# Performance work log

Hardware: AMD Instinct MI355X
Metric: run time of the kernel (lower is better)

The kernel has to match this reference:

```python
import jax, jax.numpy as jnp
import numpy as np

N_NODES = 100000
N_EDGES = 800000
NUM_GRAPHS = 64


def _lin_init(key, fan_in, fan_out):
    k1, k2 = jax.random.split(key)
    s = 1.0 / np.sqrt(fan_in)
    W = jax.random.uniform(k1, (fan_in, fan_out), jnp.float32, -s, s)
    b = jax.random.uniform(k2, (fan_out,), jnp.float32, -s, s)
    return W, b


def setup_inputs() -> dict:
    key = jax.random.key(0)
    ks = jax.random.split(key, 20)
    inp = {
        'x1': jax.random.normal(ks[0], (N_NODES, 384), jnp.float32),
        'x2': jax.random.normal(ks[1], (N_NODES, 32), jnp.float32),
        'pe': jax.random.normal(ks[2], (N_NODES, 64), jnp.float32),
        'edge_index': jax.random.randint(ks[3], (2, N_EDGES), 0, N_NODES, jnp.int32),
        'batch': jnp.sort(jax.random.randint(ks[4], (N_NODES,), 0, NUM_GRAPHS, jnp.int32)),
    }
    # parameters (fan_in, fan_out) per __init__ dims
    inp['Wc'], inp['bc'] = _lin_init(ks[5], 384, 192)     # embed_contraction
    inp['Wmf'], inp['bmf'] = _lin_init(ks[6], 192, 256)   # mpnn_feature
    inp['Wgf'], inp['bgf'] = _lin_init(ks[7], 256, 192)   # gcn_feature
    inp['Wmc'], inp['bmc'] = _lin_init(ks[8], 32, 64)     # mpnn_class
    inp['Wgc'], inp['bgc'] = _lin_init(ks[9], 64, 192)    # gcn_class
    inp['Wa1'], inp['ba1'] = _lin_init(ks[10], 192, 256)  # attention_nn[0]
    inp['Wa2'], inp['ba2'] = _lin_init(ks[11], 256, 192)  # attention_nn[2]
    inp['Wgd'], inp['bgd'] = _lin_init(ks[12], 192, 192)  # gcn_decoder
    inp['Wd1'], inp['bd1'] = _lin_init(ks[13], 192, 192)  # mpnn_decoder1
    inp['Wd2'], inp['bd2'] = _lin_init(ks[14], 192, 192)  # mpnn_decoder2
    inp['Wd3'], inp['bd3'] = _lin_init(ks[15], 192, 384)  # mpnn_decoder3
    return inp


def _mpnn(x, src, dst, W, b):
    # aggr='add': scatter-add gathered source features to targets, then Linear
    agg = jax.ops.segment_sum(x[src], dst, num_segments=N_NODES)
    return agg @ W + b


def _gcn(x, src, dst, W, b):
    # GCNConv with default self-loops and symmetric deg^-1/2 normalization
    h = x @ W
    deg = jax.ops.segment_sum(jnp.ones(src.shape[0], h.dtype), dst, num_segments=N_NODES) + 1.0
    dinv = jax.lax.rsqrt(deg)
    norm = dinv[src] * dinv[dst]
    agg = jax.ops.segment_sum(h[src] * norm[:, None], dst, num_segments=N_NODES)
    agg = agg + h * (dinv * dinv)[:, None]  # self-loop contribution
    return agg + b


def reference(x1, x2, pe, edge_index, batch,
              Wc, bc, Wmf, bmf, Wgf, bgf, Wmc, bmc, Wgc, bgc,
              Wa1, ba1, Wa2, ba2, Wgd, bgd, Wd1, bd1, Wd2, bd2, Wd3, bd3):
    src, dst = edge_index[0], edge_index[1]
    pe3 = jnp.concatenate([pe, pe, pe], axis=-1)  # [N, 192]

    # ---- encoder ----
    x1_res = jax.nn.relu(x1 @ Wc + bc)            # [N, 192]
    h = x1_res + pe3
    h = jax.nn.relu(_mpnn(h, src, dst, Wmf, bmf))  # [N, 256]
    h = jax.nn.relu(_gcn(h, src, dst, Wgf, bgf))   # [N, 192]
    c = jax.nn.relu(_mpnn(x2, src, dst, Wmc, bmc)) # [N, 64]
    c = jax.nn.relu(_gcn(c, src, dst, Wgc, bgc))   # [N, 192]
    z = h + c + x1_res

    # attentional aggregation: gate = attention_nn(z), segment softmax, weighted sum
    gate = jax.nn.relu(z @ Wa1 + ba1) @ Wa2 + ba2   # [N, 192]
    gmax = jax.ops.segment_max(gate, batch, num_segments=NUM_GRAPHS)
    e = jnp.exp(gate - gmax[batch])
    esum = jax.ops.segment_sum(e, batch, num_segments=NUM_GRAPHS)
    alpha = e / esum[batch]
    zg = jax.ops.segment_sum(alpha * z, batch, num_segments=NUM_GRAPHS)  # [B, 192]

    # ---- decoder ----
    z1 = zg[batch]                                  # broadcast graph embedding to nodes
    z1_res = jax.nn.relu(_gcn(z1, src, dst, Wgd, bgd))
    t = z1_res + pe3
    t = jax.nn.relu(_mpnn(t, src, dst, Wd1, bd1))
    t = jax.nn.relu(_mpnn(t, src, dst, Wd2, bd2)) + z1_res
    out = jax.nn.relu(_mpnn(t, src, dst, Wd3, bd3))  # [N, 384]
    return out
```

## Files before the change

kernel.cpp:

```cpp
#include <hip/hip_runtime.h>
#include <math.h>

#define N_NODES 100000
#define N_EDGES 800000
#define NGRAPH  64

typedef __attribute__((ext_vector_type(8))) __bf16 bf16x8;
typedef __attribute__((ext_vector_type(4))) float f32x4;

static __device__ __forceinline__ unsigned flip_f(float x) {
  unsigned u = __float_as_uint(x);
  return u ^ ((u & 0x80000000u) ? 0xFFFFFFFFu : 0x80000000u);
}
static __device__ __forceinline__ float unflip_f(unsigned m) {
  unsigned u = m ^ ((m & 0x80000000u) ? 0x80000000u : 0xFFFFFFFFu);
  return __uint_as_float(u);
}
static __device__ __forceinline__ unsigned short f2bf(float x) {
  unsigned u = __float_as_uint(x);
  u += 0x7fffu + ((u >> 16) & 1u);
  return (unsigned short)(u >> 16);
}
static __device__ __forceinline__ unsigned pk2(float a, float b) {
  return (unsigned)f2bf(a) | ((unsigned)f2bf(b) << 16);
}
static __device__ __forceinline__ float bf2f(unsigned short h) {
  return __uint_as_float((unsigned)h << 16);
}
static __device__ __forceinline__ void unpack8(uint4 w, float* f) {
  f[0] = __uint_as_float(w.x << 16); f[1] = __uint_as_float(w.x & 0xFFFF0000u);
  f[2] = __uint_as_float(w.y << 16); f[3] = __uint_as_float(w.y & 0xFFFF0000u);
  f[4] = __uint_as_float(w.z << 16); f[5] = __uint_as_float(w.z & 0xFFFF0000u);
  f[6] = __uint_as_float(w.w << 16); f[7] = __uint_as_float(w.w & 0xFFFF0000u);
}
static __device__ __forceinline__ uint4 pack8(const float* f) {
  uint4 w;
  w.x = pk2(f[0], f[1]); w.y = pk2(f[2], f[3]);
  w.z = pk2(f[4], f[5]); w.w = pk2(f[6], f[7]);
  return w;
}

__global__ void hist_k(const int* __restrict__ dst, int* __restrict__ cnt) {
  int e = blockIdx.x * 256 + threadIdx.x;
  if (e < N_EDGES) atomicAdd(&cnt[dst[e]], 1);
}

__global__ void dinv_k(const int* __restrict__ cnt, float* __restrict__ dinv) {
  int i = blockIdx.x * 256 + threadIdx.x;
  if (i < N_NODES) dinv[i] = rsqrtf((float)cnt[i] + 1.0f);
}

__global__ void scan_block_k(const int* __restrict__ cnt, int* __restrict__ rs,
                             int* __restrict__ bsum) {
  __shared__ int s[256];
  int t = threadIdx.x, i = blockIdx.x * 256 + t;
  int v = (i < N_NODES) ? cnt[i] : 0;
  s[t] = v; __syncthreads();
  for (int off = 1; off < 256; off <<= 1) {
    int a = (t >= off) ? s[t - off] : 0;
    __syncthreads();
    s[t] += a;
    __syncthreads();
  }
  if (i < N_NODES) rs[i] = s[t] - v;
  if (t == 255) bsum[blockIdx.x] = s[255];
}

__global__ void scan_bsum_k(int* __restrict__ bsum, int nb) {
  __shared__ int s[512];
  int t = threadIdx.x;
  int v = (t < nb) ? bsum[t] : 0;
  s[t] = v; __syncthreads();
  for (int off = 1; off < 512; off <<= 1) {
    int a = (t >= off) ? s[t - off] : 0;
    __syncthreads();
    s[t] += a;
    __syncthreads();
  }
  if (t < nb) bsum[t] = s[t] - v;
}

__global__ void scan_add_k(int* __restrict__ rs, int* __restrict__ cursor,
                           const int* __restrict__ bsum) {
  int i = blockIdx.x * 256 + threadIdx.x;
  if (i < N_NODES) {
    int r = rs[i] + bsum[i >> 8];
    rs[i] = r;
    cursor[i] = r;
  }
}

__global__ void build_k(const int* __restrict__ src, const int* __restrict__ dst,
                        int* __restrict__ cursor, int* __restrict__ srcs) {
  int e = blockIdx.x * 256 + threadIdx.x;
  if (e < N_EDGES) {
    int d = dst[e];
    int p = atomicAdd(&cursor[d], 1);
    srcs[p] = src[e];
  }
}

__global__ void graph_starts_k(const int* __restrict__ batch, int* __restrict__ gstart) {
  int g = threadIdx.x;
  if (g > NGRAPH) return;
  if (g == NGRAPH) { gstart[NGRAPH] = N_NODES; return; }
  int lo = 0, hi = N_NODES;
  while (lo < hi) {
    int mid = (lo + hi) >> 1;
    if (batch[mid] < g) lo = mid + 1; else hi = mid;
  }
  gstart[g] = lo;
}

template <typename AT, int MT, int NT, bool OUT_F32>
__global__ __launch_bounds__(256)
void gemm_t(const AT* __restrict__ A, const float* __restrict__ B,
            const float* __restrict__ bias,
            const unsigned short* __restrict__ add1,
            const unsigned short* __restrict__ add2,
            void* __restrict__ Cv, int M, int K, int F, int relu,
            const float* __restrict__ pe3src, unsigned short* __restrict__ C2) {
  constexpr int BM = 64 * MT;
  constexpr int BN = 16 * NT;
  __shared__ unsigned short As[BM * 40];
  __shared__ unsigned short Bs[BN * 40];
  const int tid = threadIdx.x;
  const int wave = tid >> 6, lane = tid & 63;
  const int quad = lane >> 4, l16 = lane & 15;
  const int row0 = blockIdx.x * BM;
  const int col0 = blockIdx.y * BN;

  f32x4 acc[MT][NT];
#pragma unroll
  for (int i = 0; i < MT; i++)
#pragma unroll
    for (int j = 0; j < NT; j++) acc[i][j] = (f32x4){0.f, 0.f, 0.f, 0.f};

  for (int k0 = 0; k0 < K; k0 += 32) {
    if (k0) __syncthreads();
    if constexpr (sizeof(AT) == 4) {
      int ar = tid >> 1, ah = (tid & 1) * 16;
      int row = row0 + ar;
      uint4 w0 = make_uint4(0, 0, 0, 0), w1 = w0;
      if (row < M) {
        const float* ap = (const float*)A + (size_t)row * K + k0 + ah;
        float4 v0 = *(const float4*)(ap + 0);
        float4 v1 = *(const float4*)(ap + 4);
        float4 v2 = *(const float4*)(ap + 8);
        float4 v3 = *(const float4*)(ap + 12);
        w0.x = pk2(v0.x, v0.y); w0.y = pk2(v0.z, v0.w);
        w0.z = pk2(v1.x, v1.y); w0.w = pk2(v1.z, v1.w);
        w1.x = pk2(v2.x, v2.y); w1.y = pk2(v2.z, v2.w);
        w1.z = pk2(v3.x, v3.y); w1.w = pk2(v3.z, v3.w);
      }
      *(uint4*)&As[ar * 40 + ah] = w0;
      *(uint4*)&As[ar * 40 + ah + 8] = w1;
    } else if constexpr (MT == 2) {
      int ar = tid >> 1, ah = (tid & 1) * 16;
      int row = row0 + ar;
      uint4 w0 = make_uint4(0, 0, 0, 0), w1 = w0;
      if (row < M) {
        const unsigned short* ap = (const unsigned short*)A + (size_t)row * K + k0 + ah;
        w0 = *(const uint4*)ap;
        w1 = *(const uint4*)(ap + 8);
      }
      *(uint4*)&As[ar * 40 + ah] = w0;
      *(uint4*)&As[ar * 40 + ah + 8] = w1;
    } else {
      int ar = tid >> 2, ap4 = (tid & 3) * 8;
      int row = row0 + ar;
      uint4 w = make_uint4(0, 0, 0, 0);
      if (row < M)
        w = *(const uint4*)((const unsigned short*)A + (size_t)row * K + k0 + ap4);
      *(uint4*)&As[ar * 40 + ap4] = w;
    }
#pragma unroll
    for (int c = 0; c < NT / 4; c++) {
      int bn = tid & 63, bkk = (tid >> 6) * 8;
      int col = col0 + c * 64 + bn;
      const float* bp = B + (size_t)(k0 + bkk) * F + col;
      uint4 w;
      w.x = pk2(bp[0 * F], bp[1 * F]); w.y = pk2(bp[2 * F], bp[3 * F]);
      w.z = pk2(bp[4 * F], bp[5 * F]); w.w = pk2(bp[6 * F], bp[7 * F]);
      *(uint4*)&Bs[(c * 64 + bn) * 40 + bkk] = w;
    }
    __syncthreads();

    bf16x8 af[MT], bfr[NT];
#pragma unroll
    for (int mt = 0; mt < MT; mt++) {
      int m = wave * (MT * 16) + mt * 16 + l16;
      af[mt] = *(bf16x8*)&As[m * 40 + quad * 8];
    }
#pragma unroll
    for (int nt = 0; nt < NT; nt++) {
      int n = nt * 16 + l16;
      bfr[nt] = *(bf16x8*)&Bs[n * 40 + quad * 8];
    }
#pragma unroll
    for (int mt = 0; mt < MT; mt++)
#pragma unroll
      for (int nt = 0; nt < NT; nt++)
        acc[mt][nt] = __builtin_amdgcn_mfma_f32_16x16x32_bf16(af[mt], bfr[nt], acc[mt][nt], 0, 0, 0);
  }

  float* Cf = (float*)Cv;
  unsigned short* Ch = (unsigned short*)Cv;
#pragma unroll
  for (int mt = 0; mt < MT; mt++) {
#pragma unroll
    for (int r = 0; r < 4; r++) {
      int row = row0 + wave * (MT * 16) + mt * 16 + quad * 4 + r;
      if (row >= M) continue;
#pragma unroll
      for (int nt = 0; nt < NT; nt++) {
        int col = col0 + nt * 16 + l16;
        float v = acc[mt][nt][r];
        if (bias) v += bias[col];
        if (relu) v = fmaxf(v, 0.f);
        size_t off = (size_t)row * F + col;
        if (add1) v += bf2f(add1[off]);
        if (add2) v += bf2f(add2[off]);
        if (OUT_F32) Cf[off] = v; else Ch[off] = f2bf(v);
        if (C2) C2[off] = f2bf(v + pe3src[(size_t)row * 64 + (col & 63)]);
      }
    }
  }
}

__global__ __launch_bounds__(256)
void gemm_kernel(const float* __restrict__ A, const float* __restrict__ B,
                 const float* __restrict__ bias, float* __restrict__ C,
                 int M, int K, int F) {
  __shared__ float Asm[16][65];
  __shared__ float Bsm[16][65];
  const int tid = threadIdx.x;
  const int tx = tid & 15, ty = tid >> 4;
  const int row0 = blockIdx.x * 64;
  const int col0 = blockIdx.y * 64;
  float acc[4][4];
#pragma unroll
  for (int i = 0; i < 4; i++)
#pragma unroll
    for (int j = 0; j < 4; j++) acc[i][j] = 0.f;

  for (int k0 = 0; k0 < K; k0 += 16) {
#pragma unroll
    for (int l = 0; l < 4; l++) {
      int idx = tid + l * 256;
      int m = idx >> 4, k = idx & 15;
      int r = row0 + m;
      Asm[k][m] = (r < M) ? A[(size_t)r * K + k0 + k] : 0.f;
    }
#pragma unroll
    for (int l = 0; l < 4; l++) {
      int idx = tid + l * 256;
      int k = idx >> 6, n = idx & 63;
      Bsm[k][n] = B[(size_t)(k0 + k) * F + col0 + n];
    }
    __syncthreads();
#pragma unroll
    for (int k = 0; k < 16; k++) {
      float a[4], b[4];
#pragma unroll
      for (int i = 0; i < 4; i++) a[i] = Asm[k][ty * 4 + i];
#pragma unroll
      for (int j = 0; j < 4; j++) b[j] = Bsm[k][tx * 4 + j];
#pragma unroll
      for (int i = 0; i < 4; i++)
#pragma unroll
        for (int j = 0; j < 4; j++) acc[i][j] += a[i] * b[j];
    }
    __syncthreads();
  }
#pragma unroll
  for (int i = 0; i < 4; i++) {
    int r = row0 + ty * 4 + i;
    if (r >= M) continue;
#pragma unroll
    for (int j = 0; j < 4; j++) {
      int c = col0 + tx * 4 + j;
      float v = acc[i][j];
      if (bias) v += bias[c];
      C[(size_t)r * F + c] = v;
    }
  }
}

template <int F>
__global__ void agg_mpnn_bf(const unsigned short* __restrict__ x, const int* __restrict__ rowstart,
                            const int* __restrict__ cnt, const int* __restrict__ srcs,
                            unsigned short* __restrict__ out) {
  constexpr int F8 = F / 8;
  int t = blockIdx.x * 256 + threadIdx.x;
  if (t >= N_NODES * F8) return;
  int i = t / F8, c = (t - i * F8) * 8;
  float a[8] = {0.f, 0.f, 0.f, 0.f, 0.f, 0.f, 0.f, 0.f};
  int e = rowstart[i], e1 = e + cnt[i];
  for (; e < e1; ++e) {
    int s = srcs[e];
    uint4 w = *(const uint4*)(x + (size_t)s * F + c);
    float f[8]; unpack8(w, f);
#pragma unroll
    for (int j = 0; j < 8; j++) a[j] += f[j];
  }
  *(uint4*)(out + (size_t)i * F + c) = pack8(a);
}

template <int F, bool RELU, bool HAS_BIAS>
__global__ void agg_gcn_bf(const unsigned short* __restrict__ x, const int* __restrict__ rowstart,
                           const int* __restrict__ cnt, const int* __restrict__ srcs,
                           const float* __restrict__ dinv, const float* __restrict__ bias,
                           unsigned short* __restrict__ out) {
  constexpr int F8 = F / 8;
  int t = blockIdx.x * 256 + threadIdx.x;
  if (t >= N_NODES * F8) return;
  int i = t / F8, c = (t - i * F8) * 8;
  float a[8] = {0.f, 0.f, 0.f, 0.f, 0.f, 0.f, 0.f, 0.f};
  int e = rowstart[i], e1 = e + cnt[i];
  for (; e < e1; ++e) {
    int s = srcs[e];
    float w = dinv[s];
    uint4 wv = *(const uint4*)(x + (size_t)s * F + c);
    float f[8]; unpack8(wv, f);
#pragma unroll
    for (int j = 0; j < 8; j++) a[j] += w * f[j];
  }
  float di = dinv[i];
  float sw = di * di;
  uint4 sv = *(const uint4*)(x + (size_t)i * F + c);
  float sf[8]; unpack8(sv, sf);
  float r[8];
#pragma unroll
  for (int j = 0; j < 8; j++) {
    float v = di * a[j] + sw * sf[j];
    if (HAS_BIAS) v += bias[c + j];
    if (RELU) v = fmaxf(v, 0.f);
    r[j] = v;
  }
  *(uint4*)(out + (size_t)i * F + c) = pack8(r);
}

__global__ void agg_x2_k(const float* __restrict__ x, const int* __restrict__ rowstart,
                         const int* __restrict__ cnt, const int* __restrict__ srcs,
                         unsigned short* __restrict__ out) {
  int t = blockIdx.x * 256 + threadIdx.x;
  if (t >= N_NODES * 8) return;
  int i = t >> 3, c = (t & 7) * 4;
  float4 acc = make_float4(0.f, 0.f, 0.f, 0.f);
  int e = rowstart[i], e1 = e + cnt[i];
  for (; e < e1; ++e) {
    int s = srcs[e];
    float4 v = *(const float4*)(x + (size_t)s * 32 + c);
    acc.x += v.x; acc.y += v.y; acc.z += v.z; acc.w += v.w;
  }
  ushort4 o;
  o.x = f2bf(acc.x); o.y = f2bf(acc.y); o.z = f2bf(acc.z); o.w = f2bf(acc.w);
  *(ushort4*)(out + (size_t)i * 32 + c) = o;
}

__global__ void agg_gcn_dec_bf(const float* __restrict__ zgW, const int* __restrict__ rowstart,
                               const int* __restrict__ cnt, const int* __restrict__ srcs,
                               const int* __restrict__ batch, const float* __restrict__ dinv,
                               const float* __restrict__ bias, unsigned short* __restrict__ out,
                               const float* __restrict__ pe, unsigned short* __restrict__ out2) {
  int t = blockIdx.x * 256 + threadIdx.x;
  if (t >= N_NODES * 24) return;
  int i = t / 24, c = (t - i * 24) * 8;
  float a[8] = {0.f, 0.f, 0.f, 0.f, 0.f, 0.f, 0.f, 0.f};
  int e = rowstart[i], e1 = e + cnt[i];
  for (; e < e1; ++e) {
    int s = srcs[e];
    float w = dinv[s];
    const float* v = zgW + (size_t)batch[s] * 192 + c;
#pragma unroll
    for (int j = 0; j < 8; j++) a[j] += w * v[j];
  }
  float di = dinv[i];
  float sw = di * di;
  const float* sv = zgW + (size_t)batch[i] * 192 + c;
  float r[8];
#pragma unroll
  for (int j = 0; j < 8; j++)
    r[j] = fmaxf(di * a[j] + sw * sv[j] + bias[c + j], 0.f);
  *(uint4*)(out + (size_t)i * 192 + c) = pack8(r);
  const float* p = pe + (size_t)i * 64 + (c & 63);
  float r2[8];
#pragma unroll
  for (int j = 0; j < 8; j++) r2[j] = r[j] + p[j];
  *(uint4*)(out2 + (size_t)i * 192 + c) = pack8(r2);
}

__global__ void init_gmax_k(unsigned* __restrict__ gmaxu) {
  int t = blockIdx.x * 256 + threadIdx.x;
  if (t < NGRAPH * 192) gmaxu[t] = 0x007FFFFFu;
}

__global__ void seg_max_k(const float* __restrict__ gate, const int* __restrict__ gstart,
                          unsigned* __restrict__ gmaxu) {
  int g = blockIdx.x, f = threadIdx.x;
  int lo = gstart[g], hi = gstart[g + 1];
  int len = hi - lo;
  if (len <= 0) return;
  int per = (len + gridDim.y - 1) / gridDim.y;
  int a = lo + blockIdx.y * per;
  int b = min(a + per, hi);
  if (a >= b) return;
  float m = -INFINITY;
  for (int i = a; i < b; i++) m = fmaxf(m, gate[(size_t)i * 192 + f]);
  atomicMax(&gmaxu[g * 192 + f], flip_f(m));
}

__global__ void seg_sum_k(const float* __restrict__ gate, const unsigned short* __restrict__ z,
                          const int* __restrict__ gstart, const unsigned* __restrict__ gmaxu,
                          float* __restrict__ esum, float* __restrict__ znum) {
  int g = blockIdx.x, f = threadIdx.x;
  int lo = gstart[g], hi = gstart[g + 1];
  int len = hi - lo;
  if (len <= 0) return;
  int per = (len + gridDim.y - 1) / gridDim.y;
  int a = lo + blockIdx.y * per;
  int b = min(a + per, hi);
  if (a >= b) return;
  float gm = unflip_f(gmaxu[g * 192 + f]);
  float se = 0.f, sz = 0.f;
  for (int i = a; i < b; i++) {
    float e = expf(gate[(size_t)i * 192 + f] - gm);
    se += e;
    sz += e * bf2f(z[(size_t)i * 192 + f]);
  }
  atomicAdd(&esum[g * 192 + f], se);
  atomicAdd(&znum[g * 192 + f], sz);
}

__global__ void zg_fin_k(const float* __restrict__ znum, const float* __restrict__ esum,
                         float* __restrict__ zg) {
  int t = blockIdx.x * 256 + threadIdx.x;
  if (t >= NGRAPH * 192) return;
  float es = esum[t];
  zg[t] = (es > 0.f) ? znum[t] / es : 0.f;
}

extern "C" void kernel_launch(void* const* d_in, const int* in_sizes, int n_in,
                              void* d_out, int out_size, void* d_ws, size_t ws_size,
                              hipStream_t stream) {
  const float* x1 = (const float*)d_in[0];
  const float* x2 = (const float*)d_in[1];
  const float* pe = (const float*)d_in[2];
  const int* ei = (const int*)d_in[3];
  const int* src = ei;
  const int* dst = ei + N_EDGES;
  const int* batch = (const int*)d_in[4];
  const float* Wc  = (const float*)d_in[5];  const float* bc  = (const float*)d_in[6];
  const float* Wmf = (const float*)d_in[7];  const float* bmf = (const float*)d_in[8];
  const float* Wgf = (const float*)d_in[9];  const float* bgf = (const float*)d_in[10];
  const float* Wmc = (const float*)d_in[11]; const float* bmc = (const float*)d_in[12];
  const float* Wgc = (const float*)d_in[13]; const float* bgc = (const float*)d_in[14];
  const float* Wa1 = (const float*)d_in[15]; const float* ba1 = (const float*)d_in[16];
  const float* Wa2 = (const float*)d_in[17]; const float* ba2 = (const float*)d_in[18];
  const float* Wgd = (const float*)d_in[19]; const float* bgd = (const float*)d_in[20];
  const float* Wd1 = (const float*)d_in[21]; const float* bd1 = (const float*)d_in[22];
  const float* Wd2 = (const float*)d_in[23]; const float* bd2 = (const float*)d_in[24];
  const float* Wd3 = (const float*)d_in[25]; const float* bd3 = (const float*)d_in[26];
  float* out = (float*)d_out;

  char* base = (char*)d_ws;
  size_t woff = 0;
  auto walloc = [&](size_t bytes) -> void* {
    void* p = base + woff;
    woff = (woff + bytes + 255) & ~(size_t)255;
    return p;
  };
  unsigned short* P0h = (unsigned short*)walloc((size_t)N_NODES * 192 * 2);
  unsigned short* P1h = (unsigned short*)walloc((size_t)N_NODES * 256 * 2);
  unsigned short* P2h = (unsigned short*)walloc((size_t)N_NODES * 192 * 2);
  unsigned short* P5a = (unsigned short*)walloc((size_t)N_NODES * 32 * 2);
  unsigned short* P5b = (unsigned short*)walloc((size_t)N_NODES * 64 * 2);
  unsigned short* P5c = (unsigned short*)walloc((size_t)N_NODES * 64 * 2);
  float* Pg   = (float*)walloc((size_t)N_NODES * 192 * 4);
  float* dinv = (float*)walloc((size_t)N_NODES * 4);
  unsigned* gmaxu = (unsigned*)walloc((size_t)NGRAPH * 192 * 4);
  float* esum = (float*)walloc((size_t)NGRAPH * 192 * 4);
  float* znum = (float*)walloc((size_t)NGRAPH * 192 * 4);
  float* zg   = (float*)walloc((size_t)NGRAPH * 192 * 4);
  float* zgW  = (float*)walloc((size_t)NGRAPH * 192 * 4);
  int* cnt      = (int*)walloc((size_t)N_NODES * 4);
  int* rowstart = (int*)walloc((size_t)N_NODES * 4);
  int* cursor   = (int*)walloc((size_t)N_NODES * 4);
  int* srcs     = (int*)walloc((size_t)N_EDGES * 4);
  int* bsum     = (int*)walloc(512 * 4);
  int* gstart   = (int*)walloc(80 * 4);

  unsigned short* P3h = (unsigned short*)d_out;
  unsigned short* P4h = (unsigned short*)((float*)d_out + (size_t)N_NODES * 192);

  const int TB = 256;
  hipMemsetAsync(cnt, 0, N_NODES * sizeof(int), stream);
  hipMemsetAsync(esum, 0, 2 * NGRAPH * 192 * sizeof(float), stream);

  hist_k<<<(N_EDGES + TB - 1) / TB, TB, 0, stream>>>(dst, cnt);
  dinv_k<<<(N_NODES + TB - 1) / TB, TB, 0, stream>>>(cnt, dinv);
  int nb = (N_NODES + 255) / 256;
  scan_block_k<<<nb, 256, 0, stream>>>(cnt, rowstart, bsum);
  scan_bsum_k<<<1, 512, 0, stream>>>(bsum, nb);
  scan_add_k<<<nb, 256, 0, stream>>>(rowstart, cursor, bsum);
  build_k<<<(N_EDGES + TB - 1) / TB, TB, 0, stream>>>(src, dst, cursor, srcs);
  graph_starts_k<<<1, 128, 0, stream>>>(batch, gstart);

  const int mb128 = (N_NODES + 127) / 128;
  const int mb64 = (N_NODES + 63) / 64;
  const int ew24 = (N_NODES * 24 + TB - 1) / TB;
  const int ew8 = (N_NODES * 8 + TB - 1) / TB;

  gemm_t<float, 2, 12, false><<<mb128, 256, 0, stream>>>(x1, Wc, bc, nullptr, nullptr, P0h, N_NODES, 384, 192, 1, pe, P1h);
  agg_mpnn_bf<192><<<ew24, TB, 0, stream>>>(P1h, rowstart, cnt, srcs, P2h);
  gemm_t<unsigned short, 1, 16, false><<<mb64, 256, 0, stream>>>(P2h, Wmf, bmf, nullptr, nullptr, P1h, N_NODES, 192, 256, 1, nullptr, nullptr);
  gemm_t<unsigned short, 2, 12, false><<<mb128, 256, 0, stream>>>(P1h, Wgf, nullptr, nullptr, nullptr, P3h, N_NODES, 256, 192, 0, nullptr, nullptr);
  agg_gcn_bf<192, true, true><<<ew24, TB, 0, stream>>>(P3h, rowstart, cnt, srcs, dinv, bgf, P4h);
  agg_x2_k<<<ew8, TB, 0, stream>>>(x2, rowstart, cnt, srcs, P5a);
  gemm_t<unsigned short, 2, 4, false><<<mb128, 256, 0, stream>>>(P5a, Wmc, bmc, nullptr, nullptr, P5b, N_NODES, 32, 64, 1, nullptr, nullptr);
  agg_gcn_bf<64, false, false><<<ew8, TB, 0, stream>>>(P5b, rowstart, cnt, srcs, dinv, nullptr, P5c);
  gemm_t<unsigned short, 2, 12, false><<<mb128, 256, 0, stream>>>(P5c, Wgc, bgc, P4h, P0h, P0h, N_NODES, 64, 192, 1, nullptr, nullptr);

  gemm_t<unsigned short, 1, 16, false><<<mb64, 256, 0, stream>>>(P0h, Wa1, ba1, nullptr, nullptr, P1h, N_NODES, 192, 256, 1, nullptr, nullptr);
  gemm_t<unsigned short, 2, 12, true><<<mb128, 256, 0, stream>>>(P1h, Wa2, ba2, nullptr, nullptr, Pg, N_NODES, 256, 192, 0, nullptr, nullptr);
  init_gmax_k<<<(NGRAPH * 192 + TB - 1) / TB, TB, 0, stream>>>(gmaxu);
  dim3 sg(NGRAPH, 16);
  seg_max_k<<<sg, 192, 0, stream>>>(Pg, gstart, gmaxu);
  seg_sum_k<<<sg, 192, 0, stream>>>(Pg, P0h, gstart, gmaxu, esum, znum);
  zg_fin_k<<<(NGRAPH * 192 + TB - 1) / TB, TB, 0, stream>>>(znum, esum, zg);
  gemm_kernel<<<dim3(1, 3), 256, 0, stream>>>(zg, Wgd, nullptr, zgW, NGRAPH, 192, 192);

  agg_gcn_dec_bf<<<ew24, TB, 0, stream>>>(zgW, rowstart, cnt, srcs, batch, dinv, bgd, P4h, pe, P2h);
  agg_mpnn_bf<192><<<ew24, TB, 0, stream>>>(P2h, rowstart, cnt, srcs, P3h);
  gemm_t<unsigned short, 2, 12, false><<<mb128, 256, 0, stream>>>(P3h, Wd1, bd1, nullptr, nullptr, P1h, N_NODES, 192, 192, 1, nullptr, nullptr);
  agg_mpnn_bf<192><<<ew24, TB, 0, stream>>>(P1h, rowstart, cnt, srcs, P2h);
  gemm_t<unsigned short, 2, 12, false><<<mb128, 256, 0, stream>>>(P2h, Wd2, bd2, P4h, nullptr, P3h, N_NODES, 192, 192, 1, nullptr, nullptr);
  agg_mpnn_bf<192><<<ew24, TB, 0, stream>>>(P3h, rowstart, cnt, srcs, P2h);
  gemm_t<unsigned short, 2, 12, true><<<dim3(mb128, 2), 256, 0, stream>>>(P2h, Wd3, bd3, nullptr, nullptr, out, N_NODES, 192, 384, 1, nullptr, nullptr);
  (void)in_sizes; (void)n_in; (void)out_size; (void)ws_size;
}
```

Baseline: 1.739 ms.

## Double-buffer GEMM LDS tiles with register prefetch and shrink row tiles

The bf16 MFMA GEMM now keeps two LDS buffers. The next K-slice is loaded into registers before computing the current slice, then written to the other buffer, so each K-step needs one barrier instead of two. All GEMM launches also switch to 64-row tiles (MT=1), and the 256-wide GEMMs split columns across two grid blocks. The aim is to hide global-load latency and raise occupancy and block count, at the cost of doubled LDS use and more register pressure from the prefetch.

```diff
diff --git a/kernel.cpp b/kernel.cpp
--- a/kernel.cpp
+++ b/kernel.cpp
@@ -122,87 +122,109 @@
             const float* __restrict__ pe3src, unsigned short* __restrict__ C2) {
   constexpr int BM = 64 * MT;
   constexpr int BN = 16 * NT;
-  __shared__ unsigned short As[BM * 40];
-  __shared__ unsigned short Bs[BN * 40];
+  constexpr int ASZ = BM * 40;
+  constexpr int BSZ = BN * 40;
+  constexpr int NB4 = NT / 4;
+  __shared__ unsigned short As[2 * ASZ];
+  __shared__ unsigned short Bs[2 * BSZ];
   const int tid = threadIdx.x;
   const int wave = tid >> 6, lane = tid & 63;
   const int quad = lane >> 4, l16 = lane & 15;
   const int row0 = blockIdx.x * BM;
   const int col0 = blockIdx.y * BN;
 
+  const int ar = (MT == 2) ? (tid >> 1) : (tid >> 2);
+  const int ac = (MT == 2) ? ((tid & 1) * 16) : ((tid & 3) * 8);
+  const int arow = row0 + ar;
+  const bool aok = arow < M;
+  const int bn = tid & 63, bkk = (tid >> 6) * 8;
+
   f32x4 acc[MT][NT];
 #pragma unroll
   for (int i = 0; i < MT; i++)
 #pragma unroll
     for (int j = 0; j < NT; j++) acc[i][j] = (f32x4){0.f, 0.f, 0.f, 0.f};
 
-  for (int k0 = 0; k0 < K; k0 += 32) {
-    if (k0) __syncthreads();
+  float4 av[MT * 2];
+  uint4 ah[MT];
+  float bv[NB4][8];
+
+  auto LOADT = [&](int k0) {
     if constexpr (sizeof(AT) == 4) {
-      int ar = tid >> 1, ah = (tid & 1) * 16;
-      int row = row0 + ar;
-      uint4 w0 = make_uint4(0, 0, 0, 0), w1 = w0;
-      if (row < M) {
-        const float* ap = (const float*)A + (size_t)row * K + k0 + ah;
-        float4 v0 = *(const float4*)(ap + 0);
-        float4 v1 = *(const float4*)(ap + 4);
-        float4 v2 = *(const float4*)(ap + 8);
-        float4 v3 = *(const float4*)(ap + 12);
-        w0.x = pk2(v0.x, v0.y); w0.y = pk2(v0.z, v0.w);
-        w0.z = pk2(v1.x, v1.y); w0.w = pk2(v1.z, v1.w);
-        w1.x = pk2(v2.x, v2.y); w1.y = pk2(v2.z, v2.w);
-        w1.z = pk2(v3.x, v3.y); w1.w = pk2(v3.z, v3.w);
+      const float* ap = (const float*)A + (size_t)arow * K + k0 + ac;
+#pragma unroll
+      for (int q = 0; q < MT * 2; q++)
+        av[q] = aok ? *(const float4*)(ap + q * 4) : make_float4(0.f, 0.f, 0.f, 0.f);
+    } else {
+      const unsigned short* ap = (const unsigned short*)A + (size_t)arow * K + k0 + ac;
+#pragma unroll
+      for (int q = 0; q < MT; q++)
+        ah[q] = aok ? *(const uint4*)(ap + q * 8) : make_uint4(0, 0, 0, 0);
+    }
+#pragma unroll
+    for (int c = 0; c < NB4; c++) {
+      const float* bp = B + (size_t)(k0 + bkk) * F + col0 + c * 64 + bn;
+#pragma unroll
+      for (int j = 0; j < 8; j++) bv[c][j] = bp[(size_t)j * F];
+    }
+  };
+
+  auto WRITET = [&](int buf) {
+    unsigned short* as = As + buf * ASZ;
+    unsigned short* bs = Bs + buf * BSZ;
+    if constexpr (sizeof(AT) == 4) {
+#pragma unroll
+      for (int q = 0; q < MT; q++) {
+        uint4 w;
+        w.x = pk2(av[2 * q].x, av[2 * q].y);
+        w.y = pk2(av[2 * q].z, av[2 * q].w);
+        w.z = pk2(av[2 * q + 1].x, av[2 * q + 1].y);
+        w.w = pk2(av[2 * q + 1].z, av[2 * q + 1].w);
+        *(uint4*)&as[ar * 40 + ac + q * 8] = w;
       }
-      *(uint4*)&As[ar * 40 + ah] = w0;
-      *(uint4*)&As[ar * 40 + ah + 8] = w1;
-    } else if constexpr (MT == 2) {
-      int ar = tid >> 1, ah = (tid & 1) * 16;
-      int row = row0 + ar;
-      uint4 w0 = make_uint4(0, 0, 0, 0), w1 = w0;
-      if (row < M) {
-        const unsigned short* ap = (const unsigned short*)A + (size_t)row * K + k0 + ah;
-        w0 = *(const uint4*)ap;
-        w1 = *(const uint4*)(ap + 8);
-      }
-      *(uint4*)&As[ar * 40 + ah] = w0;
-      *(uint4*)&As[ar * 40 + ah + 8] = w1;
     } else {
-      int ar = tid >> 2, ap4 = (tid & 3) * 8;
-      int row = row0 + ar;
-      uint4 w = make_uint4(0, 0, 0, 0);
-      if (row < M)
-        w = *(const uint4*)((const unsigned short*)A + (size_t)row * K + k0 + ap4);
-      *(uint4*)&As[ar * 40 + ap4] = w;
-    }
-#pragma unroll
-    for (int c = 0; c < NT / 4; c++) {
-      int bn = tid & 63, bkk = (tid >> 6) * 8;
-      int col = col0 + c * 64 + bn;
-      const float* bp = B + (size_t)(k0 + bkk) * F + col;
+#pragma unroll
+      for (int q = 0; q < MT; q++)
+        *(uint4*)&as[ar * 40 + ac + q * 8] = ah[q];
+    }
+#pragma unroll
+    for (int c = 0; c < NB4; c++) {
       uint4 w;
-      w.x = pk2(bp[0 * F], bp[1 * F]); w.y = pk2(bp[2 * F], bp[3 * F]);
-      w.z = pk2(bp[4 * F], bp[5 * F]); w.w = pk2(bp[6 * F], bp[7 * F]);
-      *(uint4*)&Bs[(c * 64 + bn) * 40 + bkk] = w;
-    }
-    __syncthreads();
-
-    bf16x8 af[MT], bfr[NT];
-#pragma unroll
-    for (int mt = 0; mt < MT; mt++) {
-      int m = wave * (MT * 16) + mt * 16 + l16;
-      af[mt] = *(bf16x8*)&As[m * 40 + quad * 8];
-    }
-#pragma unroll
-    for (int nt = 0; nt < NT; nt++) {
-      int n = nt * 16 + l16;
-      bfr[nt] = *(bf16x8*)&Bs[n * 40 + quad * 8];
-    }
+      w.x = pk2(bv[c][0], bv[c][1]); w.y = pk2(bv[c][2], bv[c][3]);
+      w.z = pk2(bv[c][4], bv[c][5]); w.w = pk2(bv[c][6], bv[c][7]);
+      *(uint4*)&bs[(c * 64 + bn) * 40 + bkk] = w;
+    }
+  };
+
+  auto COMPUTET = [&](int buf) {
+    const unsigned short* as = As + buf * ASZ;
+    const unsigned short* bs = Bs + buf * BSZ;
+    bf16x8 afr[MT], bfr[NT];
 #pragma unroll
     for (int mt = 0; mt < MT; mt++)
+      afr[mt] = *(const bf16x8*)&as[(wave * (MT * 16) + mt * 16 + l16) * 40 + quad * 8];
+#pragma unroll
+    for (int nt = 0; nt < NT; nt++)
+      bfr[nt] = *(const bf16x8*)&bs[(nt * 16 + l16) * 40 + quad * 8];
+#pragma unroll
+    for (int mt = 0; mt < MT; mt++)
 #pragma unroll
       for (int nt = 0; nt < NT; nt++)
-        acc[mt][nt] = __builtin_amdgcn_mfma_f32_16x16x32_bf16(af[mt], bfr[nt], acc[mt][nt], 0, 0, 0);
-  }
+        acc[mt][nt] = __builtin_amdgcn_mfma_f32_16x16x32_bf16(afr[mt], bfr[nt], acc[mt][nt], 0, 0, 0);
+  };
+
+  LOADT(0);
+  WRITET(0);
+  __syncthreads();
+  int buf = 0;
+  for (int k0 = 32; k0 < K; k0 += 32) {
+    LOADT(k0);
+    COMPUTET(buf);
+    WRITET(buf ^ 1);
+    __syncthreads();
+    buf ^= 1;
+  }
+  COMPUTET(buf);
 
   float* Cf = (float*)Cv;
   unsigned short* Ch = (unsigned short*)Cv;
@@ -507,23 +529,22 @@
   build_k<<<(N_EDGES + TB - 1) / TB, TB, 0, stream>>>(src, dst, cursor, srcs);
   graph_starts_k<<<1, 128, 0, stream>>>(batch, gstart);
 
-  const int mb128 = (N_NODES + 127) / 128;
   const int mb64 = (N_NODES + 63) / 64;
   const int ew24 = (N_NODES * 24 + TB - 1) / TB;
   const int ew8 = (N_NODES * 8 + TB - 1) / TB;
 
-  gemm_t<float, 2, 12, false><<<mb128, 256, 0, stream>>>(x1, Wc, bc, nullptr, nullptr, P0h, N_NODES, 384, 192, 1, pe, P1h);
+  gemm_t<float, 1, 12, false><<<mb64, 256, 0, stream>>>(x1, Wc, bc, nullptr, nullptr, P0h, N_NODES, 384, 192, 1, pe, P1h);
   agg_mpnn_bf<192><<<ew24, TB, 0, stream>>>(P1h, rowstart, cnt, srcs, P2h);
-  gemm_t<unsigned short, 1, 16, false><<<mb64, 256, 0, stream>>>(P2h, Wmf, bmf, nullptr, nullptr, P1h, N_NODES, 192, 256, 1, nullptr, nullptr);
-  gemm_t<unsigned short, 2, 12, false><<<mb128, 256, 0, stream>>>(P1h, Wgf, nullptr, nullptr, nullptr, P3h, N_NODES, 256, 192, 0, nullptr, nullptr);
+  gemm_t<unsigned short, 1, 8, false><<<dim3(mb64, 2), 256, 0, stream>>>(P2h, Wmf, bmf, nullptr, nullptr, P1h, N_NODES, 192, 256, 1, nullptr, nullptr);
+  gemm_t<unsigned short, 1, 12, false><<<mb64, 256, 0, stream>>>(P1h, Wgf, nullptr, nullptr, nullptr, P3h, N_NODES, 256, 192, 0, nullptr, nullptr);
   agg_gcn_bf<192, true, true><<<ew24, TB, 0, stream>>>(P3h, rowstart, cnt, srcs, dinv, bgf, P4h);
   agg_x2_k<<<ew8, TB, 0, stream>>>(x2, rowstart, cnt, srcs, P5a);
-  gemm_t<unsigned short, 2, 4, false><<<mb128, 256, 0, stream>>>(P5a, Wmc, bmc, nullptr, nullptr, P5b, N_NODES, 32, 64, 1, nullptr, nullptr);
+  gemm_t<unsigned short, 1, 4, false><<<mb64, 256, 0, stream>>>(P5a, Wmc, bmc, nullptr, nullptr, P5b, N_NODES, 32, 64, 1, nullptr, nullptr);
   agg_gcn_bf<64, false, false><<<ew8, TB, 0, stream>>>(P5b, rowstart, cnt, srcs, dinv, nullptr, P5c);
-  gemm_t<unsigned short, 2, 12, false><<<mb128, 256, 0, stream>>>(P5c, Wgc, bgc, P4h, P0h, P0h, N_NODES, 64, 192, 1, nullptr, nullptr);
-
-  gemm_t<unsigned short, 1, 16, false><<<mb64, 256, 0, stream>>>(P0h, Wa1, ba1, nullptr, nullptr, P1h, N_NODES, 192, 256, 1, nullptr, nullptr);
-  gemm_t<unsigned short, 2, 12, true><<<mb128, 256, 0, stream>>>(P1h, Wa2, ba2, nullptr, nullptr, Pg, N_NODES, 256, 192, 0, nullptr, nullptr);
+  gemm_t<unsigned short, 1, 12, false><<<mb64, 256, 0, stream>>>(P5c, Wgc, bgc, P4h, P0h, P0h, N_NODES, 64, 192, 1, nullptr, nullptr);
+
+  gemm_t<unsigned short, 1, 8, false><<<dim3(mb64, 2), 256, 0, stream>>>(P0h, Wa1, ba1, nullptr, nullptr, P1h, N_NODES, 192, 256, 1, nullptr, nullptr);
+  gemm_t<unsigned short, 1, 12, true><<<mb64, 256, 0, stream>>>(P1h, Wa2, ba2, nullptr, nullptr, Pg, N_NODES, 256, 192, 0, nullptr, nullptr);
   init_gmax_k<<<(NGRAPH * 192 + TB - 1) / TB, TB, 0, stream>>>(gmaxu);
   dim3 sg(NGRAPH, 16);
   seg_max_k<<<sg, 192, 0, stream>>>(Pg, gstart, gmaxu);
@@ -533,10 +554,10 @@
 
   agg_gcn_dec_bf<<<ew24, TB, 0, stream>>>(zgW, rowstart, cnt, srcs, batch, dinv, bgd, P4h, pe, P2h);
   agg_mpnn_bf<192><<<ew24, TB, 0, stream>>>(P2h, rowstart, cnt, srcs, P3h);
-  gemm_t<unsigned short, 2, 12, false><<<mb128, 256, 0, stream>>>(P3h, Wd1, bd1, nullptr, nullptr, P1h, N_NODES, 192, 192, 1, nullptr, nullptr);
+  gemm_t<unsigned short, 1, 12, false><<<mb64, 256, 0, stream>>>(P3h, Wd1, bd1, nullptr, nullptr, P1h, N_NODES, 192, 192, 1, nullptr, nullptr);
   agg_mpnn_bf<192><<<ew24, TB, 0, stream>>>(P1h, rowstart, cnt, srcs, P2h);
-  gemm_t<unsigned short, 2, 12, false><<<mb128, 256, 0, stream>>>(P2h, Wd2, bd2, P4h, nullptr, P3h, N_NODES, 192, 192, 1, nullptr, nullptr);
+  gemm_t<unsigned short, 1, 12, false><<<mb64, 256, 0, stream>>>(P2h, Wd2, bd2, P4h, nullptr, P3h, N_NODES, 192, 192, 1, nullptr, nullptr);
   agg_mpnn_bf<192><<<ew24, TB, 0, stream>>>(P3h, rowstart, cnt, srcs, P2h);
-  gemm_t<unsigned short, 2, 12, true><<<dim3(mb128, 2), 256, 0, stream>>>(P2h, Wd3, bd3, nullptr, nullptr, out, N_NODES, 192, 384, 1, nullptr, nullptr);
+  gemm_t<unsigned short, 1, 12, true><<<dim3(mb64, 2), 256, 0, stream>>>(P2h, Wd3, bd3, nullptr, nullptr, out, N_NODES, 192, 384, 1, nullptr, nullptr);
   (void)in_sizes; (void)n_in; (void)out_size; (void)ws_size;
 }
```

Measured after the change: 1.473 ms. -15.3%, faster.

## Keep A fragments in registers and stage only B in LDS for node GEMMs

Applied to the files above, without the earlier changes.

The GEMM kernel now loads each wave's full A row strip straight from global memory into registers as MFMA fragments, with K as a template constant. Only the weight matrix B is staged in shared memory, in large K tiles, which removes the per-32-K A shared-memory round trip and most of the barriers. Blocks drop to 64 rows with 2-3 column blocks and launch bounds of 2, trading A reuse across column blocks and more B re-conversion per block for fewer syncs and better occupancy. The larger register footprint for the A fragments, such as the K=384 fp32 input, could limit occupancy.

```diff
diff --git a/kernel.cpp b/kernel.cpp
--- a/kernel.cpp
+++ b/kernel.cpp
@@ -112,118 +112,102 @@
   gstart[g] = lo;
 }
 
-template <typename AT, int MT, int NT, bool OUT_F32>
-__global__ __launch_bounds__(256)
+template <typename AT, int K, int KT, int NT, bool OUT_F32>
+__global__ __launch_bounds__(256, 2)
 void gemm_t(const AT* __restrict__ A, const float* __restrict__ B,
             const float* __restrict__ bias,
             const unsigned short* __restrict__ add1,
             const unsigned short* __restrict__ add2,
-            void* __restrict__ Cv, int M, int K, int F, int relu,
+            void* __restrict__ Cv, int M, int F, int relu,
             const float* __restrict__ pe3src, unsigned short* __restrict__ C2) {
-  constexpr int BM = 64 * MT;
   constexpr int BN = 16 * NT;
-  __shared__ unsigned short As[BM * 40];
-  __shared__ unsigned short Bs[BN * 40];
+  constexpr int KTILES = K / KT;
+  constexpr int NSTEP = KT / 32;
+  constexpr int NFRAG = K / 32;
+  constexpr int STK = KT + 8;
+  __shared__ unsigned short Bs[BN * STK];
   const int tid = threadIdx.x;
   const int wave = tid >> 6, lane = tid & 63;
   const int quad = lane >> 4, l16 = lane & 15;
-  const int row0 = blockIdx.x * BM;
+  const int row0 = blockIdx.x * 64;
   const int col0 = blockIdx.y * BN;
-
-  f32x4 acc[MT][NT];
-#pragma unroll
-  for (int i = 0; i < MT; i++)
-#pragma unroll
-    for (int j = 0; j < NT; j++) acc[i][j] = (f32x4){0.f, 0.f, 0.f, 0.f};
-
-  for (int k0 = 0; k0 < K; k0 += 32) {
-    if (k0) __syncthreads();
-    if constexpr (sizeof(AT) == 4) {
-      int ar = tid >> 1, ah = (tid & 1) * 16;
-      int row = row0 + ar;
-      uint4 w0 = make_uint4(0, 0, 0, 0), w1 = w0;
-      if (row < M) {
-        const float* ap = (const float*)A + (size_t)row * K + k0 + ah;
-        float4 v0 = *(const float4*)(ap + 0);
-        float4 v1 = *(const float4*)(ap + 4);
-        float4 v2 = *(const float4*)(ap + 8);
-        float4 v3 = *(const float4*)(ap + 12);
-        w0.x = pk2(v0.x, v0.y); w0.y = pk2(v0.z, v0.w);
-        w0.z = pk2(v1.x, v1.y); w0.w = pk2(v1.z, v1.w);
-        w1.x = pk2(v2.x, v2.y); w1.y = pk2(v2.z, v2.w);
-        w1.z = pk2(v3.x, v3.y); w1.w = pk2(v3.z, v3.w);
+  const int arow = row0 + wave * 16 + l16;
+  const bool aok = arow < M;
+
+  float4 av[sizeof(AT) == 4 ? 2 * NFRAG : 1];
+  uint4 ah[sizeof(AT) == 4 ? 1 : NFRAG];
+  if constexpr (sizeof(AT) == 4) {
+    const float* ap = (const float*)A + (size_t)arow * K + quad * 8;
+#pragma unroll
+    for (int s = 0; s < NFRAG; s++) {
+      av[2 * s] = aok ? *(const float4*)(ap + s * 32) : make_float4(0.f, 0.f, 0.f, 0.f);
+      av[2 * s + 1] = aok ? *(const float4*)(ap + s * 32 + 4) : make_float4(0.f, 0.f, 0.f, 0.f);
+    }
+  } else {
+    const unsigned short* ap = (const unsigned short*)A + (size_t)arow * K + quad * 8;
+#pragma unroll
+    for (int s = 0; s < NFRAG; s++)
+      ah[s] = aok ? *(const uint4*)(ap + s * 32) : make_uint4(0, 0, 0, 0);
+  }
+
+  f32x4 acc[NT];
+#pragma unroll
+  for (int j = 0; j < NT; j++) acc[j] = (f32x4){0.f, 0.f, 0.f, 0.f};
+
+#pragma unroll
+  for (int kt = 0; kt < KTILES; ++kt) {
+    if (kt) __syncthreads();
+    for (int idx = tid; idx < BN * (KT / 8); idx += 256) {
+      int n = idx / (KT / 8);
+      int oct = idx - n * (KT / 8);
+      const float* bp = B + (size_t)(kt * KT + oct * 8) * F + col0 + n;
+      uint4 w;
+      w.x = pk2(bp[0 * (size_t)F], bp[1 * (size_t)F]);
+      w.y = pk2(bp[2 * (size_t)F], bp[3 * (size_t)F]);
+      w.z = pk2(bp[4 * (size_t)F], bp[5 * (size_t)F]);
+      w.w = pk2(bp[6 * (size_t)F], bp[7 * (size_t)F]);
+      *(uint4*)&Bs[n * STK + oct * 8] = w;
+    }
+    __syncthreads();
+#pragma unroll
+    for (int s = 0; s < NSTEP; ++s) {
+      const int gs = kt * NSTEP + s;
+      bf16x8 afr;
+      if constexpr (sizeof(AT) == 4) {
+        uint4 t;
+        t.x = pk2(av[2 * gs].x, av[2 * gs].y);
+        t.y = pk2(av[2 * gs].z, av[2 * gs].w);
+        t.z = pk2(av[2 * gs + 1].x, av[2 * gs + 1].y);
+        t.w = pk2(av[2 * gs + 1].z, av[2 * gs + 1].w);
+        afr = *(bf16x8*)&t;
+      } else {
+        afr = *(bf16x8*)&ah[gs];
       }
-      *(uint4*)&As[ar * 40 + ah] = w0;
-      *(uint4*)&As[ar * 40 + ah + 8] = w1;
-    } else if constexpr (MT == 2) {
-      int ar = tid >> 1, ah = (tid & 1) * 16;
-      int row = row0 + ar;
-      uint4 w0 = make_uint4(0, 0, 0, 0), w1 = w0;
-      if (row < M) {
-        const unsigned short* ap = (const unsigned short*)A + (size_t)row * K + k0 + ah;
-        w0 = *(const uint4*)ap;
-        w1 = *(const uint4*)(ap + 8);
+#pragma unroll
+      for (int nt = 0; nt < NT; nt++) {
+        bf16x8 bfr = *(const bf16x8*)&Bs[(nt * 16 + l16) * STK + s * 32 + quad * 8];
+        acc[nt] = __builtin_amdgcn_mfma_f32_16x16x32_bf16(afr, bfr, acc[nt], 0, 0, 0);
       }
-      *(uint4*)&As[ar * 40 + ah] = w0;
-      *(uint4*)&As[ar * 40 + ah + 8] = w1;
-    } else {
-      int ar = tid >> 2, ap4 = (tid & 3) * 8;
-      int row = row0 + ar;
-      uint4 w = make_uint4(0, 0, 0, 0);
-      if (row < M)
-        w = *(const uint4*)((const unsigned short*)A + (size_t)row * K + k0 + ap4);
-      *(uint4*)&As[ar * 40 + ap4] = w;
-    }
-#pragma unroll
-    for (int c = 0; c < NT / 4; c++) {
-      int bn = tid & 63, bkk = (tid >> 6) * 8;
-      int col = col0 + c * 64 + bn;
-      const float* bp = B + (size_t)(k0 + bkk) * F + col;
-      uint4 w;
-      w.x = pk2(bp[0 * F], bp[1 * F]); w.y = pk2(bp[2 * F], bp[3 * F]);
-      w.z = pk2(bp[4 * F], bp[5 * F]); w.w = pk2(bp[6 * F], bp[7 * F]);
-      *(uint4*)&Bs[(c * 64 + bn) * 40 + bkk] = w;
-    }
-    __syncthreads();
-
-    bf16x8 af[MT], bfr[NT];
-#pragma unroll
-    for (int mt = 0; mt < MT; mt++) {
-      int m = wave * (MT * 16) + mt * 16 + l16;
-      af[mt] = *(bf16x8*)&As[m * 40 + quad * 8];
-    }
-#pragma unroll
-    for (int nt = 0; nt < NT; nt++) {
-      int n = nt * 16 + l16;
-      bfr[nt] = *(bf16x8*)&Bs[n * 40 + quad * 8];
-    }
-#pragma unroll
-    for (int mt = 0; mt < MT; mt++)
-#pragma unroll
-      for (int nt = 0; nt < NT; nt++)
-        acc[mt][nt] = __builtin_amdgcn_mfma_f32_16x16x32_bf16(af[mt], bfr[nt], acc[mt][nt], 0, 0, 0);
+    }
   }
 
   float* Cf = (float*)Cv;
   unsigned short* Ch = (unsigned short*)Cv;
 #pragma unroll
-  for (int mt = 0; mt < MT; mt++) {
-#pragma unroll
-    for (int r = 0; r < 4; r++) {
-      int row = row0 + wave * (MT * 16) + mt * 16 + quad * 4 + r;
-      if (row >= M) continue;
-#pragma unroll
-      for (int nt = 0; nt < NT; nt++) {
-        int col = col0 + nt * 16 + l16;
-        float v = acc[mt][nt][r];
-        if (bias) v += bias[col];
-        if (relu) v = fmaxf(v, 0.f);
-        size_t off = (size_t)row * F + col;
-        if (add1) v += bf2f(add1[off]);
-        if (add2) v += bf2f(add2[off]);
-        if (OUT_F32) Cf[off] = v; else Ch[off] = f2bf(v);
-        if (C2) C2[off] = f2bf(v + pe3src[(size_t)row * 64 + (col & 63)]);
-      }
+  for (int r = 0; r < 4; r++) {
+    int row = row0 + wave * 16 + quad * 4 + r;
+    if (row >= M) continue;
+#pragma unroll
+    for (int nt = 0; nt < NT; nt++) {
+      int col = col0 + nt * 16 + l16;
+      float v = acc[nt][r];
+      if (bias) v += bias[col];
+      if (relu) v = fmaxf(v, 0.f);
+      size_t off = (size_t)row * F + col;
+      if (add1) v += bf2f(add1[off]);
+      if (add2) v += bf2f(add2[off]);
+      if (OUT_F32) Cf[off] = v; else Ch[off] = f2bf(v);
+      if (C2) C2[off] = f2bf(v + pe3src[(size_t)row * 64 + (col & 63)]);
     }
   }
 }
@@ -507,23 +491,22 @@
   build_k<<<(N_EDGES + TB - 1) / TB, TB, 0, stream>>>(src, dst, cursor, srcs);
   graph_starts_k<<<1, 128, 0, stream>>>(batch, gstart);
 
-  const int mb128 = (N_NODES + 127) / 128;
   const int mb64 = (N_NODES + 63) / 64;
   const int ew24 = (N_NODES * 24 + TB - 1) / TB;
   const int ew8 = (N_NODES * 8 + TB - 1) / TB;
 
-  gemm_t<float, 2, 12, false><<<mb128, 256, 0, stream>>>(x1, Wc, bc, nullptr, nullptr, P0h, N_NODES, 384, 192, 1, pe, P1h);
+  gemm_t<float, 384, 96, 12, false><<<mb64, 256, 0, stream>>>(x1, Wc, bc, nullptr, nullptr, P0h, N_NODES, 192, 1, pe, P1h);
   agg_mpnn_bf<192><<<ew24, TB, 0, stream>>>(P1h, rowstart, cnt, srcs, P2h);
-  gemm_t<unsigned short, 1, 16, false><<<mb64, 256, 0, stream>>>(P2h, Wmf, bmf, nullptr, nullptr, P1h, N_NODES, 192, 256, 1, nullptr, nullptr);
-  gemm_t<unsigned short, 2, 12, false><<<mb128, 256, 0, stream>>>(P1h, Wgf, nullptr, nullptr, nullptr, P3h, N_NODES, 256, 192, 0, nullptr, nullptr);
+  gemm_t<unsigned short, 192, 192, 8, false><<<dim3(mb64, 2), 256, 0, stream>>>(P2h, Wmf, bmf, nullptr, nullptr, P1h, N_NODES, 256, 1, nullptr, nullptr);
+  gemm_t<unsigned short, 256, 256, 6, false><<<dim3(mb64, 2), 256, 0, stream>>>(P1h, Wgf, nullptr, nullptr, nullptr, P3h, N_NODES, 192, 0, nullptr, nullptr);
   agg_gcn_bf<192, true, true><<<ew24, TB, 0, stream>>>(P3h, rowstart, cnt, srcs, dinv, bgf, P4h);
   agg_x2_k<<<ew8, TB, 0, stream>>>(x2, rowstart, cnt, srcs, P5a);
-  gemm_t<unsigned short, 2, 4, false><<<mb128, 256, 0, stream>>>(P5a, Wmc, bmc, nullptr, nullptr, P5b, N_NODES, 32, 64, 1, nullptr, nullptr);
+  gemm_t<unsigned short, 32, 32, 4, false><<<mb64, 256, 0, stream>>>(P5a, Wmc, bmc, nullptr, nullptr, P5b, N_NODES, 64, 1, nullptr, nullptr);
   agg_gcn_bf<64, false, false><<<ew8, TB, 0, stream>>>(P5b, rowstart, cnt, srcs, dinv, nullptr, P5c);
-  gemm_t<unsigned short, 2, 12, false><<<mb128, 256, 0, stream>>>(P5c, Wgc, bgc, P4h, P0h, P0h, N_NODES, 64, 192, 1, nullptr, nullptr);
-
-  gemm_t<unsigned short, 1, 16, false><<<mb64, 256, 0, stream>>>(P0h, Wa1, ba1, nullptr, nullptr, P1h, N_NODES, 192, 256, 1, nullptr, nullptr);
-  gemm_t<unsigned short, 2, 12, true><<<mb128, 256, 0, stream>>>(P1h, Wa2, ba2, nullptr, nullptr, Pg, N_NODES, 256, 192, 0, nullptr, nullptr);
+  gemm_t<unsigned short, 64, 64, 6, false><<<dim3(mb64, 2), 256, 0, stream>>>(P5c, Wgc, bgc, P4h, P0h, P0h, N_NODES, 192, 1, nullptr, nullptr);
+
+  gemm_t<unsigned short, 192, 192, 8, false><<<dim3(mb64, 2), 256, 0, stream>>>(P0h, Wa1, ba1, nullptr, nullptr, P1h, N_NODES, 256, 1, nullptr, nullptr);
+  gemm_t<unsigned short, 256, 256, 6, true><<<dim3(mb64, 2), 256, 0, stream>>>(P1h, Wa2, ba2, nullptr, nullptr, Pg, N_NODES, 192, 0, nullptr, nullptr);
   init_gmax_k<<<(NGRAPH * 192 + TB - 1) / TB, TB, 0, stream>>>(gmaxu);
   dim3 sg(NGRAPH, 16);
   seg_max_k<<<sg, 192, 0, stream>>>(Pg, gstart, gmaxu);
@@ -533,10 +516,10 @@
 
   agg_gcn_dec_bf<<<ew24, TB, 0, stream>>>(zgW, rowstart, cnt, srcs, batch, dinv, bgd, P4h, pe, P2h);
   agg_mpnn_bf<192><<<ew24, TB, 0, stream>>>(P2h, rowstart, cnt, srcs, P3h);
-  gemm_t<unsigned short, 2, 12, false><<<mb128, 256, 0, stream>>>(P3h, Wd1, bd1, nullptr, nullptr, P1h, N_NODES, 192, 192, 1, nullptr, nullptr);
+  gemm_t<unsigned short, 192, 192, 6, false><<<dim3(mb64, 2), 256, 0, stream>>>(P3h, Wd1, bd1, nullptr, nullptr, P1h, N_NODES, 192, 1, nullptr, nullptr);
   agg_mpnn_bf<192><<<ew24, TB, 0, stream>>>(P1h, rowstart, cnt, srcs, P2h);
-  gemm_t<unsigned short, 2, 12, false><<<mb128, 256, 0, stream>>>(P2h, Wd2, bd2, P4h, nullptr, P3h, N_NODES, 192, 192, 1, nullptr, nullptr);
+  gemm_t<unsigned short, 192, 192, 6, false><<<dim3(mb64, 2), 256, 0, stream>>>(P2h, Wd2, bd2, P4h, nullptr, P3h, N_NODES, 192, 1, nullptr, nullptr);
   agg_mpnn_bf<192><<<ew24, TB, 0, stream>>>(P3h, rowstart, cnt, srcs, P2h);
-  gemm_t<unsigned short, 2, 12, true><<<dim3(mb128, 2), 256, 0, stream>>>(P2h, Wd3, bd3, nullptr, nullptr, out, N_NODES, 192, 384, 1, nullptr, nullptr);
+  gemm_t<unsigned short, 192, 192, 8, true><<<dim3(mb64, 3), 256, 0, stream>>>(P2h, Wd3, bd3, nullptr, nullptr, out, N_NODES, 384, 1, nullptr, nullptr);
   (void)in_sizes; (void)n_in; (void)out_size; (void)ws_size;
 }
```

New measurement: 2.375 ms. 1.37x slower.
